# Kernel tuning notes

Measured on AMD Instinct MI355X. Metric: run time of the kernel, lower is better.

The kernel has to match this reference:

```python
import jax, jax.numpy as jnp
import numpy as np

N_NODES = 30000
N_EDGES = 480000
N_GRAPHS = 10
NODES_PER_GRAPH = 3000
MAX_RADIUS = 4.0
NUM_BASIS = 10
NUM_NEIGHBORS = 16
DIMS = [8, 288, 288, 288, 3]


def _spherical_harmonics(u):
    """e3nn-style real SH, lmax=2, 'component' normalization, on unit vectors u [E,3]."""
    x, y, z = u[:, 0], u[:, 1], u[:, 2]
    s3, s5, s15 = 3.0 ** 0.5, 5.0 ** 0.5, 15.0 ** 0.5
    return jnp.stack([
        jnp.ones_like(x),                      # l=0
        s3 * x, s3 * y, s3 * z,                # l=1
        s15 * x * z,                           # l=2
        s15 * x * y,
        s5 * (y * y - 0.5 * (x * x + z * z)),
        s15 * y * z,
        (s15 / 2.0) * (z * z - x * x),
    ], axis=1)  # [E, 9]


def _soft_one_hot_smooth_finite(r):
    """soft_one_hot_linspace(r, 0, MAX_RADIUS, NUM_BASIS, 'smooth_finite', cutoff=True)."""
    values = jnp.linspace(0.0, MAX_RADIUS, NUM_BASIS + 2)[1:-1]  # interior centers
    step = MAX_RADIUS / (NUM_BASIS + 1)
    d = (r[:, None] - values) / step
    d2 = d * d
    safe = jnp.where(d2 < 1.0, d2, 0.0)
    const = 1.14136 * float(np.exp(2.0))
    y = jnp.where(d2 < 1.0, const * jnp.exp(-1.0 / (1.0 - safe)), 0.0)
    return y * (NUM_BASIS ** 0.5)  # [E, 10]


def setup_inputs() -> dict:
    key = jax.random.key(0)
    ks = jax.random.split(key, 12)
    inp = {}
    inp['pos'] = jax.random.normal(ks[0], (N_NODES, 3), jnp.float32)
    inp['node_input'] = jax.random.normal(ks[1], (N_NODES, DIMS[0]), jnp.float32)
    inp['node_attr'] = jax.random.uniform(ks[2], (N_NODES, 1), jnp.float32)
    inp['edge_attr'] = jax.random.normal(ks[3], (N_EDGES, 1), jnp.float32)
    inp['edge_src'] = jax.random.randint(ks[4], (N_EDGES,), 0, N_NODES)
    inp['edge_dst'] = jax.random.randint(ks[5], (N_EDGES,), 0, N_NODES)
    inp['batch'] = jnp.repeat(jnp.arange(N_GRAPHS), NODES_PER_GRAPH)
    # radial MLP params (shared shapes across 4 conv layers)
    inp['fc1'] = jax.random.normal(ks[6], (4, NUM_BASIS, 100), jnp.float32) / (NUM_BASIS ** 0.5)
    inp['b1'] = jnp.zeros((4, 100), jnp.float32)
    inp['fc2'] = jax.random.normal(ks[7], (4, 100, NUM_BASIS), jnp.float32) / 10.0
    # per-layer node linear weights
    inp['W0'] = jax.random.normal(ks[8], (DIMS[0], DIMS[1]), jnp.float32) / (DIMS[0] ** 0.5)
    inp['W1'] = jax.random.normal(ks[9], (DIMS[1], DIMS[2]), jnp.float32) / (DIMS[1] ** 0.5)
    inp['W2'] = jax.random.normal(ks[10], (DIMS[2], DIMS[3]), jnp.float32) / (DIMS[2] ** 0.5)
    inp['W3'] = jax.random.normal(ks[11], (DIMS[3], DIMS[4]), jnp.float32) / (DIMS[3] ** 0.5)
    return inp


def reference(pos, node_input, node_attr, edge_attr, fc1, b1, fc2, W0, W1, W2, W3,
              edge_src, edge_dst, batch):
    edge_vec = pos[edge_src] - pos[edge_dst]               # [E,3] gather
    edge_len = jnp.linalg.norm(edge_vec, axis=1)            # [E]
    unit = edge_vec / (edge_len + 1e-12)[:, None]
    edge_sh = _spherical_harmonics(unit)                    # [E,9]
    ea = jnp.concatenate([edge_attr, edge_sh], axis=1)      # [E,10]
    emb = _soft_one_hot_smooth_finite(edge_len)             # [E,10]

    x = node_input * node_attr                               # attr-modulated input [N,8]
    Ws = [W0, W1, W2, W3]
    for l in range(4):
        rad = jax.nn.silu(emb @ fc1[l] + b1[l]) @ fc2[l]     # [E,10] radial weights
        g = jnp.sum(ea * rad, axis=1, keepdims=True)         # [E,1] edge gate (TP contraction)
        m = x[edge_src] * g                                  # [E,F] gather + per-edge product
        agg = jax.ops.segment_sum(m, edge_dst, num_segments=N_NODES)
        agg = agg / (NUM_NEIGHBORS ** 0.5)                   # scatter-reduce, e3nn normalization
        x = agg @ Ws[l]
        if l < 3:
            x = jnp.tanh(x)                                  # gate nonlinearity (simplified)
    pooled = jax.ops.segment_sum(x, batch, num_segments=N_GRAPHS)
    return pooled / (NODES_PER_GRAPH ** 0.5)                 # [10, 3]
```

## Files before the change

### kernel.cpp

```cpp
#include <hip/hip_runtime.h>
#include <math.h>

#define NN 30000
#define NE 480000
#define NG 10
#define TB 8192
#define NBS 118

typedef __attribute__((ext_vector_type(4))) float f32x4;
typedef __attribute__((ext_vector_type(8))) _Float16 half8;

__device__ __forceinline__ float h2f(ushort u) {
    _Float16 h; __builtin_memcpy(&h, &u, 2); return (float)h;
}
__device__ __forceinline__ ushort f2h(float f) {
    _Float16 h = (_Float16)f; ushort u; __builtin_memcpy(&u, &h, 2); return u;
}
__device__ __forceinline__ unsigned int pack2h(float a, float b) {
    return (unsigned int)f2h(a) | ((unsigned int)f2h(b) << 16);
}
struct F8 { float v0,v1,v2,v3,v4,v5,v6,v7; };
__device__ __forceinline__ F8 unpack8h(uint4 v) {
    F8 r;
    r.v0 = h2f((ushort)(v.x & 0xffffu)); r.v1 = h2f((ushort)(v.x >> 16));
    r.v2 = h2f((ushort)(v.y & 0xffffu)); r.v3 = h2f((ushort)(v.y >> 16));
    r.v4 = h2f((ushort)(v.z & 0xffffu)); r.v5 = h2f((ushort)(v.z >> 16));
    r.v6 = h2f((ushort)(v.w & 0xffffu)); r.v7 = h2f((ushort)(v.w >> 16));
    return r;
}
__device__ __forceinline__ float rcpf(float x) { return __builtin_amdgcn_rcpf(x); }
__device__ __forceinline__ float fast_tanh(float x) {
    return 1.0f - 2.0f * rcpf(__expf(2.0f * x) + 1.0f);
}

__global__ __launch_bounds__(256) void build_table_kernel(
    const float* __restrict__ fc1, const float* __restrict__ b1,
    const float* __restrict__ fc2, float* __restrict__ tab)
{
    int id = blockIdx.x * 256 + threadIdx.x;
    if (id >= (TB + 1) * 16) return;
    int jc = id & 3, l = (id >> 2) & 3, i = id >> 4;
    float r = (float)i * (4.0f / TB);

    float emb[10];
    const float C = 26.6692991f;
    float rr = r * 2.75f;
    #pragma unroll
    for (int k = 0; k < 10; k++) {
        float dd = rr - (float)(k + 1);
        float d2 = dd * dd;
        emb[k] = (d2 < 1.0f) ? C * __expf(-rcpf(1.0f - d2)) : 0.0f;
    }

    const float* __restrict__ F1 = fc1 + l * 1000;
    const float* __restrict__ Bv = b1 + l * 100;
    const float* __restrict__ F2 = fc2 + l * 1000;
    float q[10] = {0,0,0,0,0,0,0,0,0,0};
    int j0 = jc * 25;
    for (int j = j0; j < j0 + 25; j++) {
        float h = Bv[j];
        #pragma unroll
        for (int k = 0; k < 10; k++) h = fmaf(emb[k], F1[k * 100 + j], h);
        float s = h * rcpf(1.0f + __expf(-h));
        #pragma unroll
        for (int k = 0; k < 10; k++) q[k] = fmaf(s, F2[j * 10 + k], q[k]);
    }
    #pragma unroll
    for (int k = 0; k < 10; k++) {
        q[k] += __shfl_xor(q[k], 1);
        q[k] += __shfl_xor(q[k], 2);
    }
    if (jc == 0) {
        #pragma unroll
        for (int k = 0; k < 10; k++) tab[(size_t)i * 40 + k * 4 + l] = q[k];
    }
}

__global__ void transw_kernel(const float* __restrict__ W, ushort* __restrict__ WT)
{
    int id = blockIdx.x * 256 + threadIdx.x;
    if (id >= 288 * 288) return;
    int n = id / 288, k = id - n * 288;
    WT[id] = f2h(W[k * 288 + n]);
}

__global__ __launch_bounds__(256) void edge_g_tab_kernel(
    const float* __restrict__ pos, const float* __restrict__ edge_attr,
    const int* __restrict__ esrc, const int* __restrict__ edst,
    const int* __restrict__ eslot, const float* __restrict__ tab,
    float* __restrict__ gcsr)
{
    int e = blockIdx.x * 256 + threadIdx.x;
    if (e >= NE) return;
    int s = esrc[e], d = edst[e];
    float vx = pos[3*s+0] - pos[3*d+0];
    float vy = pos[3*s+1] - pos[3*d+1];
    float vz = pos[3*s+2] - pos[3*d+2];
    float r  = sqrtf(vx*vx + vy*vy + vz*vz);
    float inv = rcpf(r + 1e-12f);
    float ux = vx*inv, uy = vy*inv, uz = vz*inv;

    const float s3 = 1.73205081f, s5 = 2.23606798f, s15 = 3.87298335f;
    float ea[10];
    ea[0] = edge_attr[e];
    ea[1] = 1.0f;
    ea[2] = s3*ux; ea[3] = s3*uy; ea[4] = s3*uz;
    ea[5] = s15*ux*uz; ea[6] = s15*ux*uy;
    ea[7] = s5*(uy*uy - 0.5f*(ux*ux + uz*uz));
    ea[8] = s15*uy*uz;
    ea[9] = 0.5f*s15*(uz*uz - ux*ux);

    float t = r * ((float)TB / 4.0f);
    t = fminf(t, (float)TB - 0.001f);
    int i0 = (int)t;
    float f = t - (float)i0;

    const float* row0 = tab + (size_t)i0 * 40;
    const float* row1 = row0 + 40;
    float g0 = 0, g1 = 0, g2 = 0, g3 = 0;
    #pragma unroll
    for (int k = 0; k < 10; k++) {
        float4 a = *(const float4*)(row0 + k * 4);
        float4 b = *(const float4*)(row1 + k * 4);
        float w = ea[k];
        g0 = fmaf(w, fmaf(f, b.x - a.x, a.x), g0);
        g1 = fmaf(w, fmaf(f, b.y - a.y, a.y), g1);
        g2 = fmaf(w, fmaf(f, b.z - a.z, a.z), g2);
        g3 = fmaf(w, fmaf(f, b.w - a.w, a.w), g3);
    }
    int slot = eslot[e];
    gcsr[slot]          = g0 * 0.25f;
    gcsr[NE + slot]     = g1 * 0.25f;
    gcsr[2 * NE + slot] = g2 * 0.25f;
    gcsr[3 * NE + slot] = g3 * 0.25f;
}

__global__ void count_deg_kernel(const int* __restrict__ edst, int* __restrict__ deg)
{
    int e = blockIdx.x * 256 + threadIdx.x;
    if (e < NE) atomicAdd(&deg[edst[e]], 1);
}

__global__ __launch_bounds__(256) void block_sum_kernel(
    const int* __restrict__ deg, int* __restrict__ bsum)
{
    __shared__ int ws[4];
    int t = threadIdx.x;
    int idx = blockIdx.x * 256 + t;
    int v = (idx < NN) ? deg[idx] : 0;
    #pragma unroll
    for (int off = 1; off < 64; off <<= 1) v += __shfl_xor(v, off);
    if ((t & 63) == 0) ws[t >> 6] = v;
    __syncthreads();
    if (t == 0) bsum[blockIdx.x] = ws[0] + ws[1] + ws[2] + ws[3];
}

__global__ __launch_bounds__(128) void scan_bsum_kernel(
    const int* __restrict__ bsum, int* __restrict__ boff, int* __restrict__ offs)
{
    __shared__ int s[128];
    int t = threadIdx.x;
    s[t] = (t < NBS) ? bsum[t] : 0;
    __syncthreads();
    #pragma unroll
    for (int off = 1; off < 128; off <<= 1) {
        int v = (t >= off) ? s[t - off] : 0;
        __syncthreads();
        s[t] += v;
        __syncthreads();
    }
    if (t < NBS) boff[t] = (t == 0) ? 0 : s[t - 1];
    if (t == 127) offs[NN] = s[127];
}

__global__ __launch_bounds__(256) void scan_local_kernel(
    const int* __restrict__ deg, const int* __restrict__ boff,
    int* __restrict__ offs, int* __restrict__ cur)
{
    __shared__ int s[256];
    int t = threadIdx.x;
    int idx = blockIdx.x * 256 + t;
    int v = (idx < NN) ? deg[idx] : 0;
    s[t] = v;
    __syncthreads();
    #pragma unroll
    for (int off = 1; off < 256; off <<= 1) {
        int u = (t >= off) ? s[t - off] : 0;
        __syncthreads();
        s[t] += u;
        __syncthreads();
    }
    if (idx < NN) {
        int ex = boff[blockIdx.x] + s[t] - v;
        offs[idx] = ex;
        cur[idx] = ex;
    }
}

__global__ void scatter_edges_kernel(const int* __restrict__ edst, const int* __restrict__ esrc,
                                     int* __restrict__ cur, int* __restrict__ csr_src,
                                     int* __restrict__ eslot)
{
    int e = blockIdx.x * 256 + threadIdx.x;
    if (e < NE) {
        int slot = atomicAdd(&cur[edst[e]], 1);
        csr_src[slot] = esrc[e];
        eslot[e] = slot;
    }
}

__global__ void x0_kernel(const float* __restrict__ ni, const float* __restrict__ na,
                          ushort* __restrict__ x0)
{
    int n = blockIdx.x * 256 + threadIdx.x;
    if (n >= NN) return;
    float a = na[n];
    float4 v0 = *(const float4*)(ni + n * 8);
    float4 v1 = *(const float4*)(ni + n * 8 + 4);
    uint4 o;
    o.x = pack2h(v0.x * a, v0.y * a);
    o.y = pack2h(v0.z * a, v0.w * a);
    o.z = pack2h(v1.x * a, v1.y * a);
    o.w = pack2h(v1.z * a, v1.w * a);
    *(uint4*)(x0 + n * 8) = o;
}

__global__ __launch_bounds__(256) void agg8_kernel(
    const ushort* __restrict__ x0, const float* __restrict__ gc,
    const int* __restrict__ offs, const int* __restrict__ csr_src,
    ushort* __restrict__ a0)
{
    int n = blockIdx.x * 256 + threadIdx.x;
    if (n >= NN) return;
    int beg = offs[n], end = offs[n + 1];
    float a[8] = {0,0,0,0,0,0,0,0};
    for (int p = beg; p < end; p++) {
        float g = gc[p];
        int s = csr_src[p];
        F8 f = unpack8h(*(const uint4*)(x0 + (size_t)s * 8));
        a[0] = fmaf(g, f.v0, a[0]); a[1] = fmaf(g, f.v1, a[1]);
        a[2] = fmaf(g, f.v2, a[2]); a[3] = fmaf(g, f.v3, a[3]);
        a[4] = fmaf(g, f.v4, a[4]); a[5] = fmaf(g, f.v5, a[5]);
        a[6] = fmaf(g, f.v6, a[6]); a[7] = fmaf(g, f.v7, a[7]);
    }
    uint4 o;
    o.x = pack2h(a[0], a[1]);
    o.y = pack2h(a[2], a[3]);
    o.z = pack2h(a[4], a[5]);
    o.w = pack2h(a[6], a[7]);
    *(uint4*)(a0 + (size_t)n * 8) = o;
}

__global__ __launch_bounds__(256) void agg288_kernel(
    const ushort* __restrict__ xin, const float* __restrict__ gc,
    const int* __restrict__ offs, const int* __restrict__ csr_src,
    ushort* __restrict__ out)
{
    int idx = blockIdx.x * 256 + threadIdx.x;
    if (idx >= NN * 36) return;
    int n = idx / 36, c = idx - n * 36;
    int beg = offs[n], end = offs[n + 1];
    float a0=0,a1=0,a2=0,a3=0,a4=0,a5=0,a6=0,a7=0;
    const ushort* xb = xin + c * 8;
    for (int p = beg; p < end; p++) {
        float g = gc[p];
        int s = csr_src[p];
        F8 f = unpack8h(*(const uint4*)(xb + (size_t)s * 288));
        a0 = fmaf(g, f.v0, a0); a1 = fmaf(g, f.v1, a1);
        a2 = fmaf(g, f.v2, a2); a3 = fmaf(g, f.v3, a3);
        a4 = fmaf(g, f.v4, a4); a5 = fmaf(g, f.v5, a5);
        a6 = fmaf(g, f.v6, a6); a7 = fmaf(g, f.v7, a7);
    }
    uint4 o;
    o.x = pack2h(a0, a1);
    o.y = pack2h(a2, a3);
    o.z = pack2h(a4, a5);
    o.w = pack2h(a6, a7);
    *(uint4*)(out + (size_t)idx * 8) = o;
}

__global__ __launch_bounds__(256) void gemm0_kernel(
    const ushort* __restrict__ a0, const float* __restrict__ W0, ushort* __restrict__ x1)
{
    int idx = blockIdx.x * 256 + threadIdx.x;
    if (idx >= NN * 288) return;
    int n = idx / 288, c = idx - n * 288;
    F8 f = unpack8h(*(const uint4*)(a0 + (size_t)n * 8));
    float h = 0.0f;
    h = fmaf(f.v0, W0[0*288+c], h); h = fmaf(f.v1, W0[1*288+c], h);
    h = fmaf(f.v2, W0[2*288+c], h); h = fmaf(f.v3, W0[3*288+c], h);
    h = fmaf(f.v4, W0[4*288+c], h); h = fmaf(f.v5, W0[5*288+c], h);
    h = fmaf(f.v6, W0[6*288+c], h); h = fmaf(f.v7, W0[7*288+c], h);
    x1[idx] = f2h(fast_tanh(h));
}

__global__ __launch_bounds__(256) void mfma_gemm_kernel(
    const ushort* __restrict__ A, const ushort* __restrict__ BT,
    ushort* __restrict__ C, int M)
{
    __shared__ ushort As[96 * 40];
    __shared__ ushort Bs[96 * 40];
    int tid = threadIdx.x;
    int wave = tid >> 6, lane = tid & 63;
    int wr = wave >> 1, wc = wave & 1;
    int rb = blockIdx.y * 96, cb = blockIdx.x * 96;
    int kq = lane >> 4, rl = lane & 15;

    f32x4 acc[3][3];
    #pragma unroll
    for (int m = 0; m < 3; m++)
        #pragma unroll
        for (int n = 0; n < 3; n++)
            acc[m][n] = (f32x4){0.0f, 0.0f, 0.0f, 0.0f};

    for (int k0 = 0; k0 < 288; k0 += 32) {
        __syncthreads();
        for (int c = tid; c < 384; c += 256) {
            int r = c >> 2, ch = c & 3;
            int gr = rb + r;
            uint4 va = (gr < M) ? *(const uint4*)(A + (size_t)gr * 288 + k0 + ch * 8)
                                : make_uint4(0, 0, 0, 0);
            *(uint4*)&As[r * 40 + ch * 8] = va;
            uint4 vb = *(const uint4*)(BT + (size_t)(cb + r) * 288 + k0 + ch * 8);
            *(uint4*)&Bs[r * 40 + ch * 8] = vb;
        }
        __syncthreads();
        half8 a[3], b[3];
        #pragma unroll
        for (int m = 0; m < 3; m++)
            a[m] = *(const half8*)&As[(wr * 48 + m * 16 + rl) * 40 + kq * 8];
        #pragma unroll
        for (int n = 0; n < 3; n++)
            b[n] = *(const half8*)&Bs[(wc * 48 + n * 16 + rl) * 40 + kq * 8];
        #pragma unroll
        for (int m = 0; m < 3; m++)
            #pragma unroll
            for (int n = 0; n < 3; n++)
                acc[m][n] = __builtin_amdgcn_mfma_f32_16x16x32_f16(a[m], b[n], acc[m][n], 0, 0, 0);
    }
    #pragma unroll
    for (int m = 0; m < 3; m++) {
        #pragma unroll
        for (int n = 0; n < 3; n++) {
            int col = cb + wc * 48 + n * 16 + rl;
            #pragma unroll
            for (int q = 0; q < 4; q++) {
                int row = rb + wr * 48 + m * 16 + kq * 4 + q;
                if (row < M)
                    C[(size_t)row * 288 + col] = f2h(fast_tanh(acc[m][n][q]));
            }
        }
    }
}

__global__ __launch_bounds__(256) void final_kernel(
    const ushort* __restrict__ x, const float* __restrict__ W3,
    const int* __restrict__ batch, float* __restrict__ out)
{
    __shared__ float sW[864];
    __shared__ float part[NG * 3];
    int t = threadIdx.x;
    for (int i = t; i < 864; i += 256) sW[i] = W3[i];
    if (t < NG * 3) part[t] = 0.0f;
    __syncthreads();

    int n = blockIdx.x * 256 + t;
    if (n < NN) {
        float a0 = 0, a1 = 0, a2 = 0;
        const ushort* row = x + (size_t)n * 288;
        for (int k = 0; k < 288; k += 8) {
            F8 f = unpack8h(*(const uint4*)(row + k));
            a0 = fmaf(f.v0, sW[(k+0)*3+0], a0); a1 = fmaf(f.v0, sW[(k+0)*3+1], a1); a2 = fmaf(f.v0, sW[(k+0)*3+2], a2);
            a0 = fmaf(f.v1, sW[(k+1)*3+0], a0); a1 = fmaf(f.v1, sW[(k+1)*3+1], a1); a2 = fmaf(f.v1, sW[(k+1)*3+2], a2);
            a0 = fmaf(f.v2, sW[(k+2)*3+0], a0); a1 = fmaf(f.v2, sW[(k+2)*3+1], a1); a2 = fmaf(f.v2, sW[(k+2)*3+2], a2);
            a0 = fmaf(f.v3, sW[(k+3)*3+0], a0); a1 = fmaf(f.v3, sW[(k+3)*3+1], a1); a2 = fmaf(f.v3, sW[(k+3)*3+2], a2);
            a0 = fmaf(f.v4, sW[(k+4)*3+0], a0); a1 = fmaf(f.v4, sW[(k+4)*3+1], a1); a2 = fmaf(f.v4, sW[(k+4)*3+2], a2);
            a0 = fmaf(f.v5, sW[(k+5)*3+0], a0); a1 = fmaf(f.v5, sW[(k+5)*3+1], a1); a2 = fmaf(f.v5, sW[(k+5)*3+2], a2);
            a0 = fmaf(f.v6, sW[(k+6)*3+0], a0); a1 = fmaf(f.v6, sW[(k+6)*3+1], a1); a2 = fmaf(f.v6, sW[(k+6)*3+2], a2);
            a0 = fmaf(f.v7, sW[(k+7)*3+0], a0); a1 = fmaf(f.v7, sW[(k+7)*3+1], a1); a2 = fmaf(f.v7, sW[(k+7)*3+2], a2);
        }
        int g = batch[n];
        atomicAdd(&part[g*3 + 0], a0);
        atomicAdd(&part[g*3 + 1], a1);
        atomicAdd(&part[g*3 + 2], a2);
    }
    __syncthreads();
    if (t < NG * 3) {
        float v = part[t];
        if (v != 0.0f) atomicAdd(&out[t], v * 0.018257419f);
    }
}

extern "C" void kernel_launch(void* const* d_in, const int* in_sizes, int n_in,
                              void* d_out, int out_size, void* d_ws, size_t ws_size,
                              hipStream_t stream)
{
    const float* pos        = (const float*)d_in[0];
    const float* node_input = (const float*)d_in[1];
    const float* node_attr  = (const float*)d_in[2];
    const float* edge_attr  = (const float*)d_in[3];
    const int*   edge_src   = (const int*)d_in[4];
    const int*   edge_dst   = (const int*)d_in[5];
    const int*   batch      = (const int*)d_in[6];
    const float* fc1        = (const float*)d_in[7];
    const float* b1         = (const float*)d_in[8];
    const float* fc2        = (const float*)d_in[9];
    const float* W0         = (const float*)d_in[10];
    const float* W1         = (const float*)d_in[11];
    const float* W2         = (const float*)d_in[12];
    const float* W3         = (const float*)d_in[13];
    float* out = (float*)d_out;

    char* w = (char*)d_ws;
    auto alloc = [&](size_t bytes) { char* p = w; w += (bytes + 255) & ~(size_t)255; return p; };
    float*  gcsr    = (float*)alloc((size_t)NE * 4 * 4);
    int*    deg     = (int*)alloc((size_t)NN * 4);
    int*    offs    = (int*)alloc((size_t)(NN + 1) * 4);
    int*    cur     = (int*)alloc((size_t)NN * 4);
    int*    csr_src = (int*)alloc((size_t)NE * 4);
    int*    eslot   = (int*)alloc((size_t)NE * 4);
    float*  tab     = (float*)alloc((size_t)(TB + 1) * 40 * 4);
    int*    bsum    = (int*)alloc(128 * 4);
    int*    boff    = (int*)alloc(128 * 4);
    ushort* w1t     = (ushort*)alloc(288 * 288 * 2);
    ushort* w2t     = (ushort*)alloc(288 * 288 * 2);
    ushort* x0      = (ushort*)alloc((size_t)NN * 8 * 2);
    ushort* a0      = (ushort*)alloc((size_t)NN * 8 * 2);
    ushort* P       = (ushort*)alloc((size_t)NN * 288 * 2);
    ushort* Q       = (ushort*)alloc((size_t)NN * 288 * 2);

    hipMemsetAsync(deg, 0, NN * sizeof(int), stream);
    hipMemsetAsync(d_out, 0, NG * 3 * sizeof(float), stream);

    build_table_kernel<<<((TB + 1) * 16 + 255) / 256, 256, 0, stream>>>(fc1, b1, fc2, tab);
    transw_kernel<<<324, 256, 0, stream>>>(W1, w1t);
    transw_kernel<<<324, 256, 0, stream>>>(W2, w2t);
    x0_kernel<<<(NN + 255) / 256, 256, 0, stream>>>(node_input, node_attr, x0);

    count_deg_kernel<<<1875, 256, 0, stream>>>(edge_dst, deg);
    block_sum_kernel<<<NBS, 256, 0, stream>>>(deg, bsum);
    scan_bsum_kernel<<<1, 128, 0, stream>>>(bsum, boff, offs);
    scan_local_kernel<<<NBS, 256, 0, stream>>>(deg, boff, offs, cur);
    scatter_edges_kernel<<<1875, 256, 0, stream>>>(edge_dst, edge_src, cur, csr_src, eslot);

    edge_g_tab_kernel<<<1875, 256, 0, stream>>>(pos, edge_attr, edge_src, edge_dst,
                                                eslot, tab, gcsr);

    agg8_kernel<<<(NN + 255) / 256, 256, 0, stream>>>(x0, gcsr, offs, csr_src, a0);
    gemm0_kernel<<<NN * 288 / 256, 256, 0, stream>>>(a0, W0, P);
    agg288_kernel<<<(NN * 36 + 255) / 256, 256, 0, stream>>>(P, gcsr + NE, offs, csr_src, Q);
    mfma_gemm_kernel<<<dim3(3, 313), 256, 0, stream>>>(Q, w1t, P, NN);
    agg288_kernel<<<(NN * 36 + 255) / 256, 256, 0, stream>>>(P, gcsr + 2 * NE, offs, csr_src, Q);
    mfma_gemm_kernel<<<dim3(3, 313), 256, 0, stream>>>(Q, w2t, P, NN);
    agg288_kernel<<<(NN * 36 + 255) / 256, 256, 0, stream>>>(P, gcsr + 3 * NE, offs, csr_src, Q);
    final_kernel<<<(NN + 255) / 256, 256, 0, stream>>>(Q, W3, batch, out);
}
```

Measured before the change: 394.4 us.

## Stage radial MLP weights in LDS and gather edge gates via CSR permutation

The table-building kernel now copies fc1, fc2 and b1 into shared memory before evaluating the radial MLP, so the repeated weight reads hit LDS instead of global memory. The edge gate kernel writes coalesced float4 per-edge results, and a new permute kernel gathers them into CSR order using an edge-index array that the scatter step now records. This replaces four scattered writes per edge with coalesced writes plus one gathered read. The cost is an extra kernel launch, an extra buffer, and every table block reloading about 33 KB of weights into LDS, which may limit occupancy.

```diff
diff --git a/kernel.cpp b/kernel.cpp
--- a/kernel.cpp
+++ b/kernel.cpp
@@ -37,7 +37,15 @@
     const float* __restrict__ fc1, const float* __restrict__ b1,
     const float* __restrict__ fc2, float* __restrict__ tab)
 {
-    int id = blockIdx.x * 256 + threadIdx.x;
+    __shared__ float sF1[4000];
+    __shared__ float sF2[4000];
+    __shared__ float sB[400];
+    int tid = threadIdx.x;
+    for (int i = tid; i < 4000; i += 256) { sF1[i] = fc1[i]; sF2[i] = fc2[i]; }
+    for (int i = tid; i < 400; i += 256) sB[i] = b1[i];
+    __syncthreads();
+
+    int id = blockIdx.x * 256 + tid;
     if (id >= (TB + 1) * 16) return;
     int jc = id & 3, l = (id >> 2) & 3, i = id >> 4;
     float r = (float)i * (4.0f / TB);
@@ -52,9 +60,9 @@
         emb[k] = (d2 < 1.0f) ? C * __expf(-rcpf(1.0f - d2)) : 0.0f;
     }
 
-    const float* __restrict__ F1 = fc1 + l * 1000;
-    const float* __restrict__ Bv = b1 + l * 100;
-    const float* __restrict__ F2 = fc2 + l * 1000;
+    const float* __restrict__ F1 = sF1 + l * 1000;
+    const float* __restrict__ Bv = sB + l * 100;
+    const float* __restrict__ F2 = sF2 + l * 1000;
     float q[10] = {0,0,0,0,0,0,0,0,0,0};
     int j0 = jc * 25;
     for (int j = j0; j < j0 + 25; j++) {
@@ -87,8 +95,7 @@
 __global__ __launch_bounds__(256) void edge_g_tab_kernel(
     const float* __restrict__ pos, const float* __restrict__ edge_attr,
     const int* __restrict__ esrc, const int* __restrict__ edst,
-    const int* __restrict__ eslot, const float* __restrict__ tab,
-    float* __restrict__ gcsr)
+    const float* __restrict__ tab, float* __restrict__ g4)
 {
     int e = blockIdx.x * 256 + threadIdx.x;
     if (e >= NE) return;
@@ -128,11 +135,21 @@
         g2 = fmaf(w, fmaf(f, b.z - a.z, a.z), g2);
         g3 = fmaf(w, fmaf(f, b.w - a.w, a.w), g3);
     }
-    int slot = eslot[e];
-    gcsr[slot]          = g0 * 0.25f;
-    gcsr[NE + slot]     = g1 * 0.25f;
-    gcsr[2 * NE + slot] = g2 * 0.25f;
-    gcsr[3 * NE + slot] = g3 * 0.25f;
+    *(float4*)&g4[(size_t)e * 4] =
+        make_float4(g0 * 0.25f, g1 * 0.25f, g2 * 0.25f, g3 * 0.25f);
+}
+
+__global__ void permute_g_kernel(const float* __restrict__ g4, const int* __restrict__ csr,
+                                 float* __restrict__ gcsr)
+{
+    int p = blockIdx.x * 256 + threadIdx.x;
+    if (p >= NE) return;
+    int e = csr[p];
+    float4 g = *(const float4*)&g4[(size_t)e * 4];
+    gcsr[p] = g.x;
+    gcsr[NE + p] = g.y;
+    gcsr[2 * NE + p] = g.z;
+    gcsr[3 * NE + p] = g.w;
 }
 
 __global__ void count_deg_kernel(const int* __restrict__ edst, int* __restrict__ deg)
@@ -198,14 +215,14 @@
 }
 
 __global__ void scatter_edges_kernel(const int* __restrict__ edst, const int* __restrict__ esrc,
-                                     int* __restrict__ cur, int* __restrict__ csr_src,
-                                     int* __restrict__ eslot)
+                                     int* __restrict__ cur, int* __restrict__ csr,
+                                     int* __restrict__ csr_src)
 {
     int e = blockIdx.x * 256 + threadIdx.x;
     if (e < NE) {
         int slot = atomicAdd(&cur[edst[e]], 1);
+        csr[slot] = e;
         csr_src[slot] = esrc[e];
-        eslot[e] = slot;
     }
 }
 
@@ -413,12 +430,13 @@
 
     char* w = (char*)d_ws;
     auto alloc = [&](size_t bytes) { char* p = w; w += (bytes + 255) & ~(size_t)255; return p; };
+    float*  g4      = (float*)alloc((size_t)NE * 4 * 4);
     float*  gcsr    = (float*)alloc((size_t)NE * 4 * 4);
     int*    deg     = (int*)alloc((size_t)NN * 4);
     int*    offs    = (int*)alloc((size_t)(NN + 1) * 4);
     int*    cur     = (int*)alloc((size_t)NN * 4);
+    int*    csr     = (int*)alloc((size_t)NE * 4);
     int*    csr_src = (int*)alloc((size_t)NE * 4);
-    int*    eslot   = (int*)alloc((size_t)NE * 4);
     float*  tab     = (float*)alloc((size_t)(TB + 1) * 40 * 4);
     int*    bsum    = (int*)alloc(128 * 4);
     int*    boff    = (int*)alloc(128 * 4);
@@ -441,10 +459,11 @@
     block_sum_kernel<<<NBS, 256, 0, stream>>>(deg, bsum);
     scan_bsum_kernel<<<1, 128, 0, stream>>>(bsum, boff, offs);
     scan_local_kernel<<<NBS, 256, 0, stream>>>(deg, boff, offs, cur);
-    scatter_edges_kernel<<<1875, 256, 0, stream>>>(edge_dst, edge_src, cur, csr_src, eslot);
+    scatter_edges_kernel<<<1875, 256, 0, stream>>>(edge_dst, edge_src, cur, csr, csr_src);
 
     edge_g_tab_kernel<<<1875, 256, 0, stream>>>(pos, edge_attr, edge_src, edge_dst,
-                                                eslot, tab, gcsr);
+                                                tab, g4);
+    permute_g_kernel<<<1875, 256, 0, stream>>>(g4, csr, gcsr);
 
     agg8_kernel<<<(NN + 255) / 256, 256, 0, stream>>>(x0, gcsr, offs, csr_src, a0);
     gemm0_kernel<<<NN * 288 / 256, 256, 0, stream>>>(a0, W0, P);
```

Result: faster. 352.2 us (-10.7%).
